# Kernel tuning notes

Hardware: AMD Instinct MI355X
Metric: run time of the kernel (lower is better)

## Reference

```python
import jax, jax.numpy as jnp
import numpy as np

N, C, L, NUM_LAYERS = 512, 32, 1024, 3
BN_EPS = 1e-5


def setup_inputs() -> dict:
    key = jax.random.key(0)
    kx, kw, kb, kg, kbe = jax.random.split(key, 5)
    x = jax.random.normal(kx, (N, C, L), dtype=jnp.float32)
    # Per-channel, per-layer Linear weights: (C, num_layers, L_out, L_in)
    W = jax.random.normal(kw, (C, NUM_LAYERS, L, L), dtype=jnp.float32) / np.float32(np.sqrt(L))
    b = 0.01 * jax.random.normal(kb, (C, NUM_LAYERS, L), dtype=jnp.float32)
    # BatchNorm affine params for the num_layers-1 inner BN layers
    gamma = 1.0 + 0.1 * jax.random.normal(kg, (C, NUM_LAYERS - 1, L), dtype=jnp.float32)
    beta = 0.1 * jax.random.normal(kbe, (C, NUM_LAYERS - 1, L), dtype=jnp.float32)
    return {"x": x, "W": W, "b": b, "gamma": gamma, "beta": beta}


def reference(x, W, b, gamma, beta):
    """Fused per-channel MLP head.

    x: (N, C, L). For each channel c, applies num_layers Linear layers with
    ReLU + BatchNorm1d (training-mode batch stats, biased variance) between
    layers. All C channels computed as one batched GEMM per layer.
    """
    h = x
    for i in range(NUM_LAYERS):
        # batched per-channel Linear: (N,C,Lin) x (C,Lout,Lin) -> (N,C,Lout)
        h = jnp.einsum('ncl,cml->ncm', h, W[:, i]) + b[:, i][None]
        if i < NUM_LAYERS - 1:
            h = jax.nn.relu(h)
            # BatchNorm1d over the batch dim N, per (channel, feature)
            mean = jnp.mean(h, axis=0)          # (C, L)
            var = jnp.var(h, axis=0)            # biased variance, matches torch BN
            h = (h - mean) * jax.lax.rsqrt(var + BN_EPS) * gamma[:, i] + beta[:, i]
    return h
```

## Files before the change

kernel.cpp:

```cpp
#include <hip/hip_runtime.h>
#include <hip/hip_bf16.h>

#define NB 512
#define CCH 32
#define LF 1024
#define CL (CCH * LF)
#define BN_EPS 1e-5f

typedef __bf16 bf16x8 __attribute__((ext_vector_type(8)));
typedef __bf16 bf16x4 __attribute__((ext_vector_type(4)));
typedef float f32x4 __attribute__((ext_vector_type(4)));

#define QSTRIDE 1032

template <bool BNA, bool RELU>
__global__ __launch_bounds__(256, 2) void gemm_k(
    const float* __restrict__ Abase, const float* __restrict__ Wall,
    const float* __restrict__ ball, const float* __restrict__ scale,
    const float* __restrict__ shift, float* __restrict__ Out, int layer) {
  __shared__ __bf16 As[4 * QSTRIDE];
  __shared__ __bf16 Bs[4 * QSTRIDE];

  const int tid = threadIdx.x;
  const int c = blockIdx.y;
  const int mtile = blockIdx.x & 3;
  const int ntile = blockIdx.x >> 2;

  const float* A = Abase + c * LF;
  const float* Wp = Wall + (size_t)(c * 3 + layer) * LF * LF;
  const float* bias = ball + (c * 3 + layer) * LF;
  const float* scl = BNA ? scale + c * LF : nullptr;
  const float* shf = BNA ? shift + c * LF : nullptr;

  const int lane = tid & 63;
  const int wv = tid >> 6;
  const int wm = (wv & 1) * 64;
  const int wn = (wv >> 1) * 64;
  const int l15 = lane & 15;
  const int quad = lane >> 4;

  const int sr = tid >> 3;
  const int kseg = tid & 7;
  const int q = kseg >> 1;
  const int bsub = (kseg & 1) * 4;

  f32x4 acc[4][4] = {};

  for (int kt = 0; kt < LF / 32; ++kt) {
    const int k0 = kt * 32 + kseg * 4;

    f32x4 sc, sh;
    if (BNA) {
      sc = *(const f32x4*)(scl + k0);
      sh = *(const f32x4*)(shf + k0);
    }
#pragma unroll
    for (int i = 0; i < 4; ++i) {
      const int r = i * 32 + sr;
      f32x4 v = *(const f32x4*)(A + (size_t)(mtile * 128 + r) * CL + k0);
      if (BNA) v = v * sc + sh;
      bf16x4 o = {(__bf16)v.x, (__bf16)v.y, (__bf16)v.z, (__bf16)v.w};
      *(bf16x4*)&As[q * QSTRIDE + r * 8 + bsub] = o;
    }
#pragma unroll
    for (int i = 0; i < 4; ++i) {
      const int r = i * 32 + sr;
      f32x4 v = *(const f32x4*)(Wp + (size_t)(ntile * 128 + r) * LF + k0);
      bf16x4 o = {(__bf16)v.x, (__bf16)v.y, (__bf16)v.z, (__bf16)v.w};
      *(bf16x4*)&Bs[q * QSTRIDE + r * 8 + bsub] = o;
    }
    __syncthreads();

    bf16x8 af[4], bfr[4];
#pragma unroll
    for (int mi = 0; mi < 4; ++mi)
      af[mi] = *(const bf16x8*)&As[quad * QSTRIDE + (wm + mi * 16 + l15) * 8];
#pragma unroll
    for (int ni = 0; ni < 4; ++ni)
      bfr[ni] = *(const bf16x8*)&Bs[quad * QSTRIDE + (wn + ni * 16 + l15) * 8];
#pragma unroll
    for (int mi = 0; mi < 4; ++mi)
#pragma unroll
      for (int ni = 0; ni < 4; ++ni)
        acc[mi][ni] = __builtin_amdgcn_mfma_f32_16x16x32_bf16(
            af[mi], bfr[ni], acc[mi][ni], 0, 0, 0);
    __syncthreads();
  }

  float* outp = Out + (size_t)c * LF;
#pragma unroll
  for (int ni = 0; ni < 4; ++ni) {
    const int feat = ntile * 128 + wn + ni * 16 + l15;
    const float bv = bias[feat];
#pragma unroll
    for (int mi = 0; mi < 4; ++mi) {
      const int row0 = mtile * 128 + wm + mi * 16 + quad * 4;
#pragma unroll
      for (int r = 0; r < 4; ++r) {
        float v = acc[mi][ni][r] + bv;
        if (RELU) v = fmaxf(v, 0.f);
        outp[(size_t)(row0 + r) * CL + feat] = v;
      }
    }
  }
}

__global__ __launch_bounds__(256) void bn_stats(
    const float* __restrict__ H, const float* __restrict__ gamma,
    const float* __restrict__ beta, float* __restrict__ scale,
    float* __restrict__ shift, int bnlayer) {
  __shared__ float s_sum[256], s_sq[256];
  const int tid = threadIdx.x;
  const int f = tid & 63, g = tid >> 6;
  const int c = blockIdx.y;
  const int l = blockIdx.x * 64 + f;
  const float* col = H + (size_t)c * LF + l;
  float sum = 0.f, sq = 0.f;
  for (int n = g; n < NB; n += 4) {
    float v = col[(size_t)n * CL];
    sum += v;
    sq += v * v;
  }
  s_sum[tid] = sum;
  s_sq[tid] = sq;
  __syncthreads();
  if (g == 0) {
    sum = s_sum[f] + s_sum[64 + f] + s_sum[128 + f] + s_sum[192 + f];
    sq = s_sq[f] + s_sq[64 + f] + s_sq[128 + f] + s_sq[192 + f];
    const float mean = sum * (1.f / NB);
    const float var = sq * (1.f / NB) - mean * mean;
    const float rstd = rsqrtf(var + BN_EPS);
    const float ga = gamma[(size_t)(c * 2 + bnlayer) * LF + l];
    const float be = beta[(size_t)(c * 2 + bnlayer) * LF + l];
    const float sc = rstd * ga;
    scale[(size_t)c * LF + l] = sc;
    shift[(size_t)c * LF + l] = be - mean * sc;
  }
}

extern "C" void kernel_launch(void* const* d_in, const int* in_sizes, int n_in,
                              void* d_out, int out_size, void* d_ws,
                              size_t ws_size, hipStream_t stream) {
  const float* x = (const float*)d_in[0];
  const float* W = (const float*)d_in[1];
  const float* b = (const float*)d_in[2];
  const float* gamma = (const float*)d_in[3];
  const float* beta = (const float*)d_in[4];
  float* out = (float*)d_out;

  float* scale0 = (float*)d_ws;
  float* shift0 = scale0 + CCH * LF;
  float* scale1 = shift0 + CCH * LF;
  float* shift1 = scale1 + CCH * LF;
  float* h2 = shift1 + CCH * LF;

  const dim3 blk(256);
  const dim3 ggrid(32, 32);
  const dim3 sgrid(16, 32);

  gemm_k<false, true><<<ggrid, blk, 0, stream>>>(x, W, b, nullptr, nullptr, out, 0);
  bn_stats<<<sgrid, blk, 0, stream>>>(out, gamma, beta, scale0, shift0, 0);
  gemm_k<true, true><<<ggrid, blk, 0, stream>>>(out, W, b, scale0, shift0, h2, 1);
  bn_stats<<<sgrid, blk, 0, stream>>>(h2, gamma, beta, scale1, shift1, 1);
  gemm_k<true, false><<<ggrid, blk, 0, stream>>>(h2, W, b, scale1, shift1, out, 2);
}
```

Before: 943.0 us.

## Pre-convert inputs to bf16 and load GEMM tiles with direct global-to-LDS DMA

Adds kernels that convert W and x to bf16 up front. The GEMMs now stream bf16 tiles straight into shared memory with global_load_lds instead of loading fp32, converting and storing through registers. Intermediate activations are stored as bf16, and BatchNorm is applied in place by a fused stats-plus-normalize kernel rather than being folded into the next GEMM's A load. This cuts register work and global traffic in the GEMMs, but adds a full pass over W (about 400MB read) on every call and an extra read/write pass over the activations.

```diff
diff --git a/kernel.cpp b/kernel.cpp
--- a/kernel.cpp
+++ b/kernel.cpp
@@ -8,29 +8,40 @@
 #define BN_EPS 1e-5f
 
 typedef __bf16 bf16x8 __attribute__((ext_vector_type(8)));
-typedef __bf16 bf16x4 __attribute__((ext_vector_type(4)));
 typedef float f32x4 __attribute__((ext_vector_type(4)));
 
-#define QSTRIDE 1032
+__device__ __forceinline__ void gload16(const __bf16* g, __bf16* l) {
+  __builtin_amdgcn_global_load_lds(
+      (const __attribute__((address_space(1))) unsigned int*)g,
+      (__attribute__((address_space(3))) unsigned int*)l, 16, 0, 0);
+}
 
-template <bool BNA, bool RELU>
-__global__ __launch_bounds__(256, 2) void gemm_k(
-    const float* __restrict__ Abase, const float* __restrict__ Wall,
-    const float* __restrict__ ball, const float* __restrict__ scale,
-    const float* __restrict__ shift, float* __restrict__ Out, int layer) {
-  __shared__ __bf16 As[4 * QSTRIDE];
-  __shared__ __bf16 Bs[4 * QSTRIDE];
+__global__ __launch_bounds__(256) void cvt_bf16(const float* __restrict__ s,
+                                                __bf16* __restrict__ d) {
+  const size_t i = ((size_t)blockIdx.x * 256 + threadIdx.x) * 8;
+  f32x4 a = *(const f32x4*)(s + i);
+  f32x4 b = *(const f32x4*)(s + i + 4);
+  bf16x8 o = {(__bf16)a.x, (__bf16)a.y, (__bf16)a.z, (__bf16)a.w,
+              (__bf16)b.x, (__bf16)b.y, (__bf16)b.z, (__bf16)b.w};
+  *(bf16x8*)(d + i) = o;
+}
+
+template <bool RELU, bool BF16OUT>
+__global__ __launch_bounds__(256, 3) void gemm_dma(
+    const __bf16* __restrict__ Abf, const __bf16* __restrict__ Wall,
+    const float* __restrict__ ball, void* __restrict__ outv, int layer) {
+  __shared__ __bf16 As[4096];
+  __shared__ __bf16 Bs[4096];
 
   const int tid = threadIdx.x;
   const int c = blockIdx.y;
   const int mtile = blockIdx.x & 3;
   const int ntile = blockIdx.x >> 2;
+  const int m0 = mtile * 128, n0 = ntile * 128;
 
-  const float* A = Abase + c * LF;
-  const float* Wp = Wall + (size_t)(c * 3 + layer) * LF * LF;
-  const float* bias = ball + (c * 3 + layer) * LF;
-  const float* scl = BNA ? scale + c * LF : nullptr;
-  const float* shf = BNA ? shift + c * LF : nullptr;
+  const __bf16* A = Abf + (size_t)c * LF;
+  const __bf16* Wp = Wall + (size_t)(c * 3 + layer) * LF * LF;
+  const float* bias = ball + (size_t)(c * 3 + layer) * LF;
 
   const int lane = tid & 63;
   const int wv = tid >> 6;
@@ -39,45 +50,37 @@
   const int l15 = lane & 15;
   const int quad = lane >> 4;
 
-  const int sr = tid >> 3;
-  const int kseg = tid & 7;
-  const int q = kseg >> 1;
-  const int bsub = (kseg & 1) * 4;
+  const __bf16 *pa[2], *pb[2];
+  __bf16 *la[2], *lb[2];
+#pragma unroll
+  for (int j = 0; j < 2; ++j) {
+    const int s = wv * 128 + j * 64 + lane;
+    const int q = s >> 7, r = s & 127;
+    pa[j] = A + (size_t)(m0 + r) * CL + q * 8;
+    pb[j] = Wp + (size_t)(n0 + r) * LF + q * 8;
+    la[j] = As + (wv * 128 + j * 64) * 8;
+    lb[j] = Bs + (wv * 128 + j * 64) * 8;
+  }
 
   f32x4 acc[4][4] = {};
 
   for (int kt = 0; kt < LF / 32; ++kt) {
-    const int k0 = kt * 32 + kseg * 4;
-
-    f32x4 sc, sh;
-    if (BNA) {
-      sc = *(const f32x4*)(scl + k0);
-      sh = *(const f32x4*)(shf + k0);
-    }
 #pragma unroll
-    for (int i = 0; i < 4; ++i) {
-      const int r = i * 32 + sr;
-      f32x4 v = *(const f32x4*)(A + (size_t)(mtile * 128 + r) * CL + k0);
-      if (BNA) v = v * sc + sh;
-      bf16x4 o = {(__bf16)v.x, (__bf16)v.y, (__bf16)v.z, (__bf16)v.w};
-      *(bf16x4*)&As[q * QSTRIDE + r * 8 + bsub] = o;
-    }
-#pragma unroll
-    for (int i = 0; i < 4; ++i) {
-      const int r = i * 32 + sr;
-      f32x4 v = *(const f32x4*)(Wp + (size_t)(ntile * 128 + r) * LF + k0);
-      bf16x4 o = {(__bf16)v.x, (__bf16)v.y, (__bf16)v.z, (__bf16)v.w};
-      *(bf16x4*)&Bs[q * QSTRIDE + r * 8 + bsub] = o;
+    for (int j = 0; j < 2; ++j) {
+      gload16(pa[j], la[j]);
+      gload16(pb[j], lb[j]);
+      pa[j] += 32;
+      pb[j] += 32;
     }
     __syncthreads();
 
     bf16x8 af[4], bfr[4];
 #pragma unroll
     for (int mi = 0; mi < 4; ++mi)
-      af[mi] = *(const bf16x8*)&As[quad * QSTRIDE + (wm + mi * 16 + l15) * 8];
+      af[mi] = *(const bf16x8*)&As[(quad * 128 + wm + mi * 16 + l15) * 8];
 #pragma unroll
     for (int ni = 0; ni < 4; ++ni)
-      bfr[ni] = *(const bf16x8*)&Bs[quad * QSTRIDE + (wn + ni * 16 + l15) * 8];
+      bfr[ni] = *(const bf16x8*)&Bs[(quad * 128 + wn + ni * 16 + l15) * 8];
 #pragma unroll
     for (int mi = 0; mi < 4; ++mi)
 #pragma unroll
@@ -87,54 +90,62 @@
     __syncthreads();
   }
 
-  float* outp = Out + (size_t)c * LF;
 #pragma unroll
   for (int ni = 0; ni < 4; ++ni) {
-    const int feat = ntile * 128 + wn + ni * 16 + l15;
+    const int feat = n0 + wn + ni * 16 + l15;
     const float bv = bias[feat];
 #pragma unroll
     for (int mi = 0; mi < 4; ++mi) {
-      const int row0 = mtile * 128 + wm + mi * 16 + quad * 4;
+      const int row0 = m0 + wm + mi * 16 + quad * 4;
 #pragma unroll
       for (int r = 0; r < 4; ++r) {
         float v = acc[mi][ni][r] + bv;
         if (RELU) v = fmaxf(v, 0.f);
-        outp[(size_t)(row0 + r) * CL + feat] = v;
+        if (BF16OUT)
+          ((__bf16*)outv)[(size_t)c * LF + (size_t)(row0 + r) * CL + feat] =
+              (__bf16)v;
+        else
+          ((float*)outv)[(size_t)c * LF + (size_t)(row0 + r) * CL + feat] = v;
       }
     }
   }
 }
 
-__global__ __launch_bounds__(256) void bn_stats(
-    const float* __restrict__ H, const float* __restrict__ gamma,
-    const float* __restrict__ beta, float* __restrict__ scale,
-    float* __restrict__ shift, int bnlayer) {
-  __shared__ float s_sum[256], s_sq[256];
+__global__ __launch_bounds__(256, 4) void bn_fused(__bf16* __restrict__ H,
+                                                   const float* __restrict__ gam,
+                                                   const float* __restrict__ bet,
+                                                   int bnl) {
+  __shared__ float ssum[256], ssq[256], sscale[64], sshift[64];
   const int tid = threadIdx.x;
   const int f = tid & 63, g = tid >> 6;
   const int c = blockIdx.y;
   const int l = blockIdx.x * 64 + f;
-  const float* col = H + (size_t)c * LF + l;
+  __bf16* col = H + (size_t)c * LF + l;
+
   float sum = 0.f, sq = 0.f;
   for (int n = g; n < NB; n += 4) {
-    float v = col[(size_t)n * CL];
+    float v = (float)col[(size_t)n * CL];
     sum += v;
     sq += v * v;
   }
-  s_sum[tid] = sum;
-  s_sq[tid] = sq;
+  ssum[tid] = sum;
+  ssq[tid] = sq;
   __syncthreads();
-  if (g == 0) {
-    sum = s_sum[f] + s_sum[64 + f] + s_sum[128 + f] + s_sum[192 + f];
-    sq = s_sq[f] + s_sq[64 + f] + s_sq[128 + f] + s_sq[192 + f];
+  if (tid < 64) {
+    sum = ssum[f] + ssum[64 + f] + ssum[128 + f] + ssum[192 + f];
+    sq = ssq[f] + ssq[64 + f] + ssq[128 + f] + ssq[192 + f];
     const float mean = sum * (1.f / NB);
     const float var = sq * (1.f / NB) - mean * mean;
     const float rstd = rsqrtf(var + BN_EPS);
-    const float ga = gamma[(size_t)(c * 2 + bnlayer) * LF + l];
-    const float be = beta[(size_t)(c * 2 + bnlayer) * LF + l];
-    const float sc = rstd * ga;
-    scale[(size_t)c * LF + l] = sc;
-    shift[(size_t)c * LF + l] = be - mean * sc;
+    const float sc = rstd * gam[(size_t)(c * 2 + bnl) * LF + l];
+    sscale[f] = sc;
+    sshift[f] = bet[(size_t)(c * 2 + bnl) * LF + l] - mean * sc;
+  }
+  __syncthreads();
+  const float sc = sscale[f], sh = sshift[f];
+  for (int n = g; n < NB; n += 4) {
+    float v = (float)col[(size_t)n * CL];
+    col[(size_t)n * CL] = (__bf16)(v * sc + sh);
   }
 }
 
@@ -148,19 +159,21 @@
   const float* beta = (const float*)d_in[4];
   float* out = (float*)d_out;
 
-  float* scale0 = (float*)d_ws;
-  float* shift0 = scale0 + CCH * LF;
-  float* scale1 = shift0 + CCH * LF;
-  float* shift1 = scale1 + CCH * LF;
-  float* h2 = shift1 + CCH * LF;
+  __bf16* Wbf = (__bf16*)d_ws;
+  __bf16* xbf = Wbf + (size_t)CCH * 3 * LF * LF;
+  __bf16* h1 = xbf + (size_t)NB * CL;
+  __bf16* h2 = h1 + (size_t)NB * CL;
 
   const dim3 blk(256);
-  const dim3 ggrid(32, 32);
-  const dim3 sgrid(16, 32);
+  const dim3 ggrid(32, CCH);
+  const dim3 bgrid(16, CCH);
 
-  gemm_k<false, true><<<ggrid, blk, 0, stream>>>(x, W, b, nullptr, nullptr, out, 0);
-  bn_stats<<<sgrid, blk, 0, stream>>>(out, gamma, beta, scale0, shift0, 0);
-  gemm_k<true, true><<<ggrid, blk, 0, stream>>>(out, W, b, scale0, shift0, h2, 1);
-  bn_stats<<<sgrid, blk, 0, stream>>>(h2, gamma, beta, scale1, shift1, 1);
-  gemm_k<true, false><<<ggrid, blk, 0, stream>>>(h2, W, b, scale1, shift1, out, 2);
+  cvt_bf16<<<dim3((CCH * 3 * LF * LF) / (8 * 256)), blk, 0, stream>>>(W, Wbf);
+  cvt_bf16<<<dim3(((size_t)NB * CL) / (8 * 256)), blk, 0, stream>>>(x, xbf);
+
+  gemm_dma<true, true><<<ggrid, blk, 0, stream>>>(xbf, Wbf, b, h1, 0);
+  bn_fused<<<bgrid, blk, 0, stream>>>(h1, gamma, beta, 0);
+  gemm_dma<true, true><<<ggrid, blk, 0, stream>>>(h1, Wbf, b, h2, 1);
+  bn_fused<<<bgrid, blk, 0, stream>>>(h2, gamma, beta, 1);
+  gemm_dma<false, false><<<ggrid, blk, 0, stream>>>(h2, Wbf, b, out, 2);
 }
```

After: 980.9 us. 4.0% more time.
